# Kernel optimization log

Measured on AMD Instinct MI355X. Metric: run time of the kernel, lower is better.

The kernel has to match this reference:

```python
import jax, jax.numpy as jnp
import numpy as np

B, S, D, H, FF = 4, 1024, 1024, 16, 4096
HD = D // H
SCALE = float(np.sqrt(HD))
LAMBDA_MIN = 0.5
LAMBDA_MAX = 0.5
EPS = 1e-5


def _layernorm(x, g, b):
    mu = jnp.mean(x, axis=-1, keepdims=True)
    var = jnp.mean(jnp.square(x - mu), axis=-1, keepdims=True)
    return (x - mu) * jax.lax.rsqrt(var + EPS) * g + b


def _qbnn_layer(h, W, bW, J, lam_base, g, be):
    # s_prev = tanh(h); h_tilde = h W + b; delta_j = (sum_i s_prev_i J_ij) * tanh(h_tilde)_j
    s_prev = jnp.tanh(h)
    h_tilde = h @ W + bW
    s_raw = jnp.tanh(h_tilde)
    delta = (s_prev @ J) * s_raw
    lam_n = jax.nn.sigmoid(lam_base)
    dynamic_factor = 0.5  # eval mode, call_count=0 -> 0.5+0.5*sin(0)
    lam_eff = LAMBDA_MIN + (LAMBDA_MAX - LAMBDA_MIN) * (lam_n * 0.7 + dynamic_factor * 0.3)
    h_hat = h_tilde + lam_eff * delta
    return jax.nn.gelu(_layernorm(h_hat, g, be), approximate=False)


def setup_inputs() -> dict:
    key = jax.random.key(0)
    ks = jax.random.split(key, 24)
    f32 = jnp.float32
    lin = lambda k, i, o: jax.random.normal(k, (i, o), f32) / np.sqrt(i)
    inp = {
        'x': jax.random.normal(ks[0], (B, S, D), f32),
        # attention projections (stored as [in, out]; y = x @ W + b)
        'wq': lin(ks[1], D, D), 'bq': jnp.zeros((D,), f32),
        'wk': lin(ks[2], D, D), 'bk': jnp.zeros((D,), f32),
        'wv': lin(ks[3], D, D), 'bv': jnp.zeros((D,), f32),
        'wo': lin(ks[4], D, D), 'bo': jnp.zeros((D,), f32),
        'J_attn': jax.random.normal(ks[5], (H, HD, HD), f32) * 0.02,
        'lambda_attn': jnp.asarray(0.5, f32),
        'g_attn': jnp.ones((D,), f32), 'b_attn': jnp.zeros((D,), f32),
        # ffn layer 1 (D -> FF)
        'W1': lin(ks[6], D, FF), 'b1': jnp.zeros((FF,), f32),
        'J1': jax.random.normal(ks[7], (D, FF), f32) * 0.02,
        'lam1': jnp.asarray(0.5, f32),
        'g1': jnp.ones((FF,), f32), 'be1': jnp.zeros((FF,), f32),
        # ffn layer 2 (FF -> D)
        'W2': lin(ks[8], FF, D), 'b2': jnp.zeros((D,), f32),
        'J2': jax.random.normal(ks[9], (FF, D), f32) * 0.02,
        'lam2': jnp.asarray(0.5, f32),
        'g2': jnp.ones((D,), f32), 'be2': jnp.zeros((D,), f32),
        # ffn pre-norm
        'g_ffn': jnp.ones((D,), f32), 'b_ffn': jnp.zeros((D,), f32),
    }
    return inp


def reference(x, wq, bq, wk, bk, wv, bv, wo, bo, J_attn, lambda_attn, g_attn, b_attn,
              W1, b1, J1, lam1, g1, be1, W2, b2, J2, lam2, g2, be2, g_ffn, b_ffn):
    # --- attention (pre-norm) ---
    xn = _layernorm(x, g_attn, b_attn)
    split = lambda t: t.reshape(B, S, H, HD).transpose(0, 2, 1, 3)  # bshd -> bhsd
    Q = split(xn @ wq + bq)
    K = split(xn @ wk + bk)
    V = split(xn @ wv + bv)
    scores = jnp.einsum('bhid,bhjd->bhij', Q, K) / SCALE
    tQJ = jnp.einsum('bhid,hde->bhie', jnp.tanh(Q), J_attn)
    delta = jnp.einsum('bhie,bhje->bhij', tQJ, jnp.tanh(K))
    probs = jax.nn.softmax(scores + lambda_attn * delta, axis=-1)
    attn = jnp.einsum('bhij,bhjd->bhid', probs, V)
    attn = attn.transpose(0, 2, 1, 3).reshape(B, S, D) @ wo + bo
    x = x + attn
    # --- QBNN FFN (pre-norm) ---
    h = _layernorm(x, g_ffn, b_ffn)
    h = _qbnn_layer(h, W1, b1, J1, lam1, g1, be1)
    h = _qbnn_layer(h, W2, b2, J2, lam2, g2, be2)
    return x + h
```

## Files before the change

### kernel.cpp

```cpp
#include <hip/hip_runtime.h>
#include <cmath>

typedef unsigned short u16;
typedef unsigned int   u32;
typedef short bhalf8 __attribute__((ext_vector_type(8)));
typedef float fx4    __attribute__((ext_vector_type(4)));

#define B_   4
#define S_   1024
#define D_   1024
#define H_   16
#define HD_  64
#define FF_  4096
#define NTOK (B_*S_)
#define QKVW 3072

__device__ __forceinline__ float b2f(u16 u) {
    u32 x = ((u32)u) << 16;
    return __uint_as_float(x);
}
__device__ __forceinline__ u16 f2b(float f) {
    u32 u = __float_as_uint(f);
    u32 r = (u + 0x7fffu + ((u >> 16) & 1u)) >> 16;
    return (u16)r;
}
__device__ __forceinline__ float ftanh(float x) {
    float e = __expf(2.f * x);
    return 1.f - 2.f / (e + 1.f);
}

#define GLDS16(g, l) __builtin_amdgcn_global_load_lds( \
    (const __attribute__((address_space(1))) void*)(g), \
    (__attribute__((address_space(3))) void*)(l), 16, 0, 0)

template <int N> __device__ __forceinline__ void waitvm() {
    if constexpr (N == 8) asm volatile("s_waitcnt vmcnt(8)" ::: "memory");
    else if constexpr (N == 6) asm volatile("s_waitcnt vmcnt(6)" ::: "memory");
    else if constexpr (N == 4) asm volatile("s_waitcnt vmcnt(4)" ::: "memory");
    else if constexpr (N == 3) asm volatile("s_waitcnt vmcnt(3)" ::: "memory");
    else if constexpr (N == 2) asm volatile("s_waitcnt vmcnt(2)" ::: "memory");
    else asm volatile("s_waitcnt vmcnt(0)" ::: "memory");
}

__device__ __forceinline__ void tile_swz(int gx, int gy, int& bx, int& by) {
    int bid = blockIdx.x;
    int nwg = gx * gy;
    if (((nwg | gy) & 7) == 0) {
        int chunk = nwg >> 3;
        int wg = (bid & 7) * chunk + (bid >> 3);
        int tps = gx << 3;
        int sup = wg / tps, rem = wg % tps;
        bx = rem >> 3;
        by = (sup << 3) + (rem & 7);
    } else {
        bx = bid % gx; by = bid / gx;
    }
}

__global__ __launch_bounds__(256) void cvt_t_k(const float* __restrict__ w0, const float* __restrict__ w1,
                                               const float* __restrict__ w2, const float* __restrict__ w3,
                                               const float* __restrict__ W1p, const float* __restrict__ J1p,
                                               const float* __restrict__ W2p, const float* __restrict__ J2p,
                                               u16* __restrict__ dst) {
    __shared__ u16 L[64][65];
    int bid = blockIdx.x, tid = threadIdx.x;
    const float* src; size_t dbase; int Kd, Nd, tk, tn;
    if (bid < 1024)      { int m = bid >> 8, t = bid & 255;
                           src = m == 0 ? w0 : m == 1 ? w1 : m == 2 ? w2 : w3;
                           dbase = (size_t)m << 20; Kd = 1024; Nd = 1024; tk = t >> 4; tn = t & 15; }
    else if (bid < 2048) { int t = bid - 1024; src = W1p; dbase = (size_t)4  << 20; Kd = 1024; Nd = 4096; tk = t >> 6; tn = t & 63; }
    else if (bid < 3072) { int t = bid - 2048; src = J1p; dbase = (size_t)8  << 20; Kd = 1024; Nd = 4096; tk = t >> 6; tn = t & 63; }
    else if (bid < 4096) { int t = bid - 3072; src = W2p; dbase = (size_t)12 << 20; Kd = 4096; Nd = 1024; tk = t >> 4; tn = t & 15; }
    else                 { int t = bid - 4096; src = J2p; dbase = (size_t)16 << 20; Kd = 4096; Nd = 1024; tk = t >> 4; tn = t & 15; }
    int k0 = tk * 64, n0 = tn * 64;
    int r = tid >> 2, c4 = (tid & 3) * 16;
    #pragma unroll
    for (int p = 0; p < 4; ++p) {
        float4 v = *(const float4*)&src[(size_t)(k0 + r) * Nd + n0 + c4 + p * 4];
        L[r][c4 + p * 4 + 0] = f2b(v.x);
        L[r][c4 + p * 4 + 1] = f2b(v.y);
        L[r][c4 + p * 4 + 2] = f2b(v.z);
        L[r][c4 + p * 4 + 3] = f2b(v.w);
    }
    __syncthreads();
    u16 o[16];
    #pragma unroll
    for (int j = 0; j < 16; ++j) o[j] = L[c4 + j][r];
    *(uint4*)&dst[dbase + (size_t)(n0 + r) * Kd + k0 + c4]     = *(uint4*)&o[0];
    *(uint4*)&dst[dbase + (size_t)(n0 + r) * Kd + k0 + c4 + 8] = *(uint4*)&o[8];
}

__global__ __launch_bounds__(256) void tanh_k(const u16* __restrict__ in, u16* __restrict__ outb) {
    size_t idx = ((size_t)blockIdx.x * 256 + threadIdx.x) * 8;
    uint4 v = *(const uint4*)&in[idx];
    const u16* p = (const u16*)&v;
    u16 o[8];
    #pragma unroll
    for (int j = 0; j < 8; ++j) o[j] = f2b(ftanh(b2f(p[j])));
    *(uint4*)&outb[idx] = *(uint4*)o;
}

template <int BM, int BN, int WM, int WN, int EPI, bool SEG>
__global__ __launch_bounds__(512, 2) void gemmP(const u16* __restrict__ A,
                                                const u16* __restrict__ Bt,
                                                const float* __restrict__ bA,
                                                const float* __restrict__ bB,
                                                const float* __restrict__ bC,
                                                const float* __restrict__ resid,
                                                void* __restrict__ Cout,
                                                int M, int N, int K) {
    constexpr int IA = BM / 128;
    constexpr int IB = BN / 128;
    constexpr int NWN = BN / WN;
    constexpr int FM = WM / 16, FN = WN / 16;
    __shared__ u16 As[3][BM * 32];
    __shared__ u16 Bs[3][BN * 32];

    const int tid = threadIdx.x;
    const int w = tid >> 6, ln = tid & 63;
    const int q = ln >> 4, mr = ln & 15;
    const int wmi = w / NWN, wni = w % NWN;
    int bx, by;
    tile_swz(N / BN, M / BM, bx, by);
    const int m0 = by * BM, n0 = bx * BN;

    const int lr = ln >> 2;
    const int sc = 8 * ((ln & 3) ^ ((ln >> 3) & 3));
    const int qx8 = 8 * (q ^ ((mr >> 1) & 3));

    const u16* aA[IA];
    const u16* aB[IB];
    #pragma unroll
    for (int i = 0; i < IA; ++i)
        aA[i] = A + (size_t)(m0 + 16 * (w + 8 * i) + lr) * K + sc;
    #pragma unroll
    for (int i = 0; i < IB; ++i)
        aB[i] = Bt + (size_t)(n0 + 16 * (w + 8 * i) + lr) * K + sc;

    fx4 acc[FM][FN];
    #pragma unroll
    for (int i = 0; i < FM; ++i)
        #pragma unroll
        for (int j = 0; j < FN; ++j) acc[i][j] = (fx4){0.f, 0.f, 0.f, 0.f};

#define GP_STAGE(slot, kk) do { \
        _Pragma("unroll") \
        for (int i = 0; i < IA; ++i) GLDS16(aA[i] + (kk), &As[slot][(16 * (w + 8 * i)) * 32]); \
        _Pragma("unroll") \
        for (int i = 0; i < IB; ++i) GLDS16(aB[i] + (kk), &Bs[slot][(16 * (w + 8 * i)) * 32]); \
    } while (0)

    const int NT = K >> 5;
    GP_STAGE(0, 0);
    GP_STAGE(1, 32);
    int sl = 0, st = 2;
    for (int t = 0; t < NT; ++t) {
        if (t + 2 < NT) {
            GP_STAGE(st, (t + 2) << 5);
            waitvm<2 * (IA + IB)>();
        } else if (t + 1 < NT) {
            waitvm<IA + IB>();
        } else {
            waitvm<0>();
        }
        __builtin_amdgcn_sched_barrier(0);
        __builtin_amdgcn_s_barrier();
        __builtin_amdgcn_sched_barrier(0);

        bhalf8 afr[FM], bfr[FN];
        const u16* Ap = &As[sl][0];
        const u16* Bp = &Bs[sl][0];
        #pragma unroll
        for (int fm = 0; fm < FM; ++fm)
            afr[fm] = *(const bhalf8*)&Ap[(wmi * WM + fm * 16 + mr) * 32 + qx8];
        #pragma unroll
        for (int fn = 0; fn < FN; ++fn)
            bfr[fn] = *(const bhalf8*)&Bp[(wni * WN + fn * 16 + mr) * 32 + qx8];
        asm volatile("s_waitcnt lgkmcnt(0)" ::: "memory");
        __builtin_amdgcn_sched_barrier(0);
        __builtin_amdgcn_s_barrier();
        __builtin_amdgcn_sched_barrier(0);

        __builtin_amdgcn_s_setprio(1);
        #pragma unroll
        for (int fm = 0; fm < FM; ++fm)
            #pragma unroll
            for (int fn = 0; fn < FN; ++fn)
                acc[fm][fn] = __builtin_amdgcn_mfma_f32_16x16x32_bf16(afr[fm], bfr[fn], acc[fm][fn], 0, 0, 0);
        __builtin_amdgcn_s_setprio(0);

        sl = sl == 2 ? 0 : sl + 1;
        st = st == 2 ? 0 : st + 1;
    }
#undef GP_STAGE

    #pragma unroll
    for (int fn = 0; fn < FN; ++fn) {
        int col = n0 + wni * WN + fn * 16 + mr;
        float bs;
        if (SEG) {
            const float* bp = col < 1024 ? bA : (col < 2048 ? bB : bC);
            bs = bp[col & 1023];
        } else {
            bs = bA ? bA[col] : 0.f;
        }
        #pragma unroll
        for (int fm = 0; fm < FM; ++fm) {
            #pragma unroll
            for (int r = 0; r < 4; ++r) {
                int row    = m0 + wmi * WM + fm * 16 + q * 4 + r;
                size_t idx = (size_t)row * N + col;
                float v    = acc[fm][fn][r] + bs;
                if (EPI == 0) {
                    ((u16*)Cout)[idx] = f2b(v);
                } else if (EPI == 1) {
                    ((float*)Cout)[idx] = v + resid[idx];
                } else {
                    float ht = b2f(((u16*)Cout)[idx]);
                    ((u16*)Cout)[idx] = f2b(ht + 0.5f * v * ftanh(ht));
                }
            }
        }
    }
}

__global__ __launch_bounds__(256) void ln_k(const float* __restrict__ xin,
                                            const float* __restrict__ g,
                                            const float* __restrict__ bb,
                                            u16* __restrict__ out, int W) {
    __shared__ float red[8], red2[8], stats[2];
    int row = blockIdx.x, tid = threadIdx.x;
    float s = 0.f, ss = 0.f;
    for (int c = tid; c < W; c += 256) {
        float v = xin[(size_t)row * W + c];
        s += v; ss += v * v;
    }
    #pragma unroll
    for (int off = 32; off; off >>= 1) { s += __shfl_xor(s, off); ss += __shfl_xor(ss, off); }
    int wave = tid >> 6, lane = tid & 63;
    if (lane == 0) { red[wave] = s; red2[wave] = ss; }
    __syncthreads();
    if (tid == 0) {
        float S = 0.f, SS = 0.f;
        for (int w2 = 0; w2 < 4; ++w2) { S += red[w2]; SS += red2[w2]; }
        float mu = S / W;
        stats[0] = mu;
        stats[1] = rsqrtf(SS / W - mu * mu + 1e-5f);
    }
    __syncthreads();
    float mu = stats[0], rs = stats[1];
    for (int c = tid; c < W; c += 256)
        out[(size_t)row * W + c] = f2b((xin[(size_t)row * W + c] - mu) * rs * g[c] + bb[c]);
}

template <bool RES, bool OUT_F32>
__global__ __launch_bounds__(256) void lngelu_k(const u16* __restrict__ u,
                                                const float* __restrict__ g,
                                                const float* __restrict__ be,
                                                const float* __restrict__ resid,
                                                void* __restrict__ out, int W) {
    __shared__ float ub[4096];
    __shared__ float red[8], red2[8], stats[2];
    int row = blockIdx.x, tid = threadIdx.x;
    float s = 0.f, ss = 0.f;
    for (int c = tid; c < W; c += 256) {
        float v = b2f(u[(size_t)row * W + c]);
        ub[c] = v; s += v; ss += v * v;
    }
    #pragma unroll
    for (int off = 32; off; off >>= 1) { s += __shfl_xor(s, off); ss += __shfl_xor(ss, off); }
    int wave = tid >> 6, lane = tid & 63;
    if (lane == 0) { red[wave] = s; red2[wave] = ss; }
    __syncthreads();
    if (tid == 0) {
        float S = 0.f, SS = 0.f;
        for (int w2 = 0; w2 < 4; ++w2) { S += red[w2]; SS += red2[w2]; }
        float mu = S / W;
        stats[0] = mu;
        stats[1] = rsqrtf(SS / W - mu * mu + 1e-5f);
    }
    __syncthreads();
    float mu = stats[0], rs = stats[1];
    for (int c = tid; c < W; c += 256) {
        float v = (ub[c] - mu) * rs * g[c] + be[c];
        float y = 0.5f * v * (1.f + erff(v * 0.70710678118654752f));
        if (RES) y += resid[(size_t)row * W + c];
        if (OUT_F32) ((float*)out)[(size_t)row * W + c] = y;
        else         ((u16*)out)[(size_t)row * W + c] = f2b(y);
    }
}

__global__ __launch_bounds__(256) void aug_q_k(const u16* __restrict__ QKV,
                                               const float* __restrict__ J,
                                               const float* __restrict__ lamp,
                                               u16* __restrict__ QA) {
    __shared__ float Jl[64][68];
    __shared__ float Tq[64][65];
    int blk = blockIdx.x;
    int bh = blk >> 4, st = blk & 15;
    int b = bh >> 4, h = bh & 15;
    int s0 = st * 64;
    int tid = threadIdx.x;
    float lam = lamp[0];

    for (int i = tid; i < 4096; i += 256)
        Jl[i >> 6][i & 63] = J[h * 4096 + i];
    for (int i = tid; i < 4096; i += 256) {
        int r = i >> 6, c = i & 63;
        float v  = b2f(QKV[(size_t)(b * S_ + s0 + r) * QKVW + h * 64 + c]);
        Tq[r][c] = ftanh(v);
        QA[((size_t)(bh * S_ + s0 + r)) * 128 + c] = f2b(v * 0.125f);
    }
    __syncthreads();

    int r = tid >> 2, c0 = (tid & 3) * 16;
    float acc[16];
    #pragma unroll
    for (int j = 0; j < 16; ++j) acc[j] = 0.f;
    for (int k = 0; k < 64; ++k) {
        float a = Tq[r][k];
        #pragma unroll
        for (int j4 = 0; j4 < 4; ++j4) {
            float4 jv = *(const float4*)&Jl[k][c0 + j4 * 4];
            acc[j4 * 4 + 0] += a * jv.x;
            acc[j4 * 4 + 1] += a * jv.y;
            acc[j4 * 4 + 2] += a * jv.z;
            acc[j4 * 4 + 3] += a * jv.w;
        }
    }
    size_t orow = ((size_t)(bh * S_ + s0 + r)) * 128 + 64 + c0;
    #pragma unroll
    for (int j = 0; j < 16; ++j) QA[orow + j] = f2b(lam * acc[j]);
}

__global__ __launch_bounds__(256) void aug_k_k(const u16* __restrict__ QKV,
                                               u16* __restrict__ KA) {
    int idx = blockIdx.x * 256 + threadIdx.x;
    int d = idx & (D_ - 1);
    int bs = idx >> 10;
    int h = d >> 6, hd = d & 63;
    int b = bs >> 10, si = bs & (S_ - 1);
    u16 v      = QKV[(size_t)bs * QKVW + 1024 + d];
    size_t row = (size_t)((b * H_ + h) * S_ + si);
    KA[row * 128 + hd]      = v;
    KA[row * 128 + 64 + hd] = f2b(ftanh(b2f(v)));
}

#define QS_STRIDE 136
#define PS_STRIDE 72
__global__ __launch_bounds__(256) void attn_k(const u16* __restrict__ QA,
                                              const u16* __restrict__ KA,
                                              const u16* __restrict__ QKV,
                                              u16* __restrict__ out) {
    __shared__ u16 Qs[64 * QS_STRIDE];
    __shared__ u16 Ks[64 * QS_STRIDE];
    __shared__ u16 Vt[64 * PS_STRIDE];
    __shared__ u16 Ps[4 * 16 * PS_STRIDE];

    const int tid  = threadIdx.x;
    const int w    = tid >> 6, lane = tid & 63;
    const int q    = lane >> 4, mr = lane & 15;
    const int bh   = blockIdx.x >> 4;
    const int qt   = blockIdx.x & 15;
    const int b    = bh >> 4, h = bh & 15;

    #pragma unroll
    for (int p = 0; p < 4; ++p) {
        int idx = p * 2048 + tid * 8;
        int row = idx >> 7, col = idx & 127;
        uint4 v4 = *(const uint4*)&QA[((size_t)(bh * S_ + qt * 64 + row)) * 128 + col];
        *(uint4*)&Qs[row * QS_STRIDE + col] = v4;
    }

    fx4 zero = {0.f, 0.f, 0.f, 0.f};
    fx4 O[4] = {zero, zero, zero, zero};
    float m[4]  = {-3e38f, -3e38f, -3e38f, -3e38f};
    float l[4]  = {0.f, 0.f, 0.f, 0.f};

    for (int kt = 0; kt < 16; ++kt) {
        #pragma unroll
        for (int p = 0; p < 4; ++p) {
            int idx = p * 2048 + tid * 8;
            int row = idx >> 7, col = idx & 127;
            uint4 v4 = *(const uint4*)&KA[((size_t)(bh * S_ + kt * 64 + row)) * 128 + col];
            *(uint4*)&Ks[row * QS_STRIDE + col] = v4;
        }
        #pragma unroll
        for (int p = 0; p < 2; ++p) {
            int idx = p * 2048 + tid * 8;
            int key = idx >> 6, d0 = idx & 63;
            uint4 v4 = *(const uint4*)&QKV[((size_t)(b * S_ + kt * 64 + key)) * QKVW + 2048 + h * 64 + d0];
            const u16* vp = (const u16*)&v4;
            #pragma unroll
            for (int j = 0; j < 8; ++j) Vt[(d0 + j) * PS_STRIDE + key] = vp[j];
        }
        __syncthreads();

        fx4 St[4] = {zero, zero, zero, zero};
        bhalf8 afr[4];
        #pragma unroll
        for (int ks = 0; ks < 4; ++ks)
            afr[ks] = *(const bhalf8*)&Qs[(w * 16 + mr) * QS_STRIDE + ks * 32 + q * 8];
        __builtin_amdgcn_s_setprio(1);
        #pragma unroll
        for (int nt = 0; nt < 4; ++nt) {
            #pragma unroll
            for (int ks = 0; ks < 4; ++ks) {
                bhalf8 bf = *(const bhalf8*)&Ks[(nt * 16 + mr) * QS_STRIDE + ks * 32 + q * 8];
                St[nt] = __builtin_amdgcn_mfma_f32_16x16x32_bf16(afr[ks], bf, St[nt], 0, 0, 0);
            }
        }
        __builtin_amdgcn_s_setprio(0);

        float alpha[4];
        #pragma unroll
        for (int r = 0; r < 4; ++r) {
            float mx = fmaxf(fmaxf(St[0][r], St[1][r]), fmaxf(St[2][r], St[3][r]));
            #pragma unroll
            for (int off = 8; off; off >>= 1) mx = fmaxf(mx, __shfl_xor(mx, off));
            float nm = fmaxf(m[r], mx);
            alpha[r] = __expf(m[r] - nm);
            m[r] = nm;
            float ps = 0.f;
            #pragma unroll
            for (int nt = 0; nt < 4; ++nt) {
                float p = __expf(St[nt][r] - nm);
                St[nt][r] = p;
                ps += p;
            }
            #pragma unroll
            for (int off = 8; off; off >>= 1) ps += __shfl_xor(ps, off);
            l[r] = l[r] * alpha[r] + ps;
        }
        #pragma unroll
        for (int nt = 0; nt < 4; ++nt) {
            #pragma unroll
            for (int r = 0; r < 4; ++r) {
                Ps[(w * 16 + q * 4 + r) * PS_STRIDE + nt * 16 + mr] = f2b(St[nt][r]);
                O[nt][r] *= alpha[r];
            }
        }

        __builtin_amdgcn_s_setprio(1);
        #pragma unroll
        for (int ks = 0; ks < 2; ++ks) {
            bhalf8 pa = *(const bhalf8*)&Ps[(w * 16 + mr) * PS_STRIDE + ks * 32 + q * 8];
            #pragma unroll
            for (int nt = 0; nt < 4; ++nt) {
                bhalf8 bf = *(const bhalf8*)&Vt[(nt * 16 + mr) * PS_STRIDE + ks * 32 + q * 8];
                O[nt] = __builtin_amdgcn_mfma_f32_16x16x32_bf16(pa, bf, O[nt], 0, 0, 0);
            }
        }
        __builtin_amdgcn_s_setprio(0);
        __syncthreads();
    }

    #pragma unroll
    for (int nt = 0; nt < 4; ++nt) {
        int d = nt * 16 + mr;
        #pragma unroll
        for (int r = 0; r < 4; ++r) {
            int row = qt * 64 + w * 16 + q * 4 + r;
            out[((size_t)(b * S_ + row)) * D_ + h * 64 + d] = f2b(O[nt][r] / l[r]);
        }
    }
}

extern "C" void kernel_launch(void* const* d_in, const int* in_sizes, int n_in,
                              void* d_out, int out_size, void* d_ws, size_t ws_size,
                              hipStream_t stream) {
    const float* x      = (const float*)d_in[0];
    const float* wq     = (const float*)d_in[1];
    const float* bq     = (const float*)d_in[2];
    const float* wk     = (const float*)d_in[3];
    const float* bk     = (const float*)d_in[4];
    const float* wv     = (const float*)d_in[5];
    const float* bv     = (const float*)d_in[6];
    const float* wo     = (const float*)d_in[7];
    const float* bo     = (const float*)d_in[8];
    const float* Jattn  = (const float*)d_in[9];
    const float* lamA   = (const float*)d_in[10];
    const float* g_attn = (const float*)d_in[11];
    const float* b_attn = (const float*)d_in[12];
    const float* W1     = (const float*)d_in[13];
    const float* b1     = (const float*)d_in[14];
    const float* J1     = (const float*)d_in[15];
    const float* g1     = (const float*)d_in[17];
    const float* be1    = (const float*)d_in[18];
    const float* W2     = (const float*)d_in[19];
    const float* b2     = (const float*)d_in[20];
    const float* J2     = (const float*)d_in[21];
    const float* g2     = (const float*)d_in[23];
    const float* be2    = (const float*)d_in[24];
    const float* g_ffn  = (const float*)d_in[25];
    const float* b_ffn  = (const float*)d_in[26];
    float* out = (float*)d_out;
    (void)in_sizes; (void)n_in; (void)out_size; (void)ws_size;

    char* wsp = (char*)d_ws;
    const size_t MB = 1u << 20;
    u16* WB = (u16*)(wsp);
    const u16* qkvT = WB;
    const u16* woT  = WB + ((size_t)3 << 20);
    const u16* W1T  = WB + ((size_t)4 << 20);
    const u16* J1T  = WB + ((size_t)8 << 20);
    const u16* W2T  = WB + ((size_t)12 << 20);
    const u16* J2T  = WB + ((size_t)16 << 20);
    u16*   XN   = (u16*)(wsp + 40 * MB);
    u16*   AT   = (u16*)(wsp + 40 * MB);
    u16*   U2   = (u16*)(wsp + 40 * MB);
    u16*   QKVb = (u16*)(wsp + 48 * MB);
    u16*   Hb   = (u16*)(wsp + 48 * MB);
    float* X2   = (float*)(wsp + 56 * MB);
    u16*   QA   = (u16*)(wsp + 72 * MB);
    u16*   KA   = (u16*)(wsp + 88 * MB);
    u16*   U1   = (u16*)(wsp + 72 * MB);

    dim3 blk(256), blk5(512);
    cvt_t_k<<<5120, blk, 0, stream>>>(wq, wk, wv, wo, W1, J1, W2, J2, WB);
    ln_k<<<NTOK, blk, 0, stream>>>(x, g_attn, b_attn, XN, D_);
    gemmP<128, 256, 64, 64, 0, true><<<(QKVW / 256) * (NTOK / 128), blk5, 0, stream>>>(
        XN, qkvT, bq, bk, bv, nullptr, QKVb, NTOK, QKVW, D_);
    aug_q_k<<<B_ * H_ * (S_ / 64), blk, 0, stream>>>(QKVb, Jattn, lamA, QA);
    aug_k_k<<<(NTOK * D_) / 256, blk, 0, stream>>>(QKVb, KA);
    attn_k<<<B_ * H_ * (S_ / 64), blk, 0, stream>>>(QA, KA, QKVb, AT);
    gemmP<128, 128, 64, 32, 1, false><<<(D_ / 128) * (NTOK / 128), blk5, 0, stream>>>(
        AT, woT, bo, nullptr, nullptr, x, X2, NTOK, D_, D_);
    ln_k<<<NTOK, blk, 0, stream>>>(X2, g_ffn, b_ffn, Hb, D_);
    gemmP<256, 256, 128, 64, 0, false><<<(FF_ / 256) * (NTOK / 256), blk5, 0, stream>>>(
        Hb, W1T, b1, nullptr, nullptr, nullptr, U1, NTOK, FF_, D_);
    tanh_k<<<(NTOK * D_) / 2048, blk, 0, stream>>>(Hb, Hb);
    gemmP<256, 256, 128, 64, 2, false><<<(FF_ / 256) * (NTOK / 256), blk5, 0, stream>>>(
        Hb, J1T, nullptr, nullptr, nullptr, nullptr, U1, NTOK, FF_, D_);
    lngelu_k<false, false><<<NTOK, blk, 0, stream>>>(U1, g1, be1, nullptr, U1, FF_);
    gemmP<128, 128, 64, 32, 0, false><<<(D_ / 128) * (NTOK / 128), blk5, 0, stream>>>(
        U1, W2T, b2, nullptr, nullptr, nullptr, U2, NTOK, D_, FF_);
    tanh_k<<<(NTOK * FF_) / 2048, blk, 0, stream>>>(U1, U1);
    gemmP<128, 128, 64, 32, 2, false><<<(D_ / 128) * (NTOK / 128), blk5, 0, stream>>>(
        U1, J2T, nullptr, nullptr, nullptr, nullptr, U2, NTOK, D_, FF_);
    lngelu_k<true, true><<<NTOK, blk, 0, stream>>>(U2, g2, be2, X2, out, D_);
}
```

Measured before the change: 716.7 us.

## Pipeline attention K/V loads, pre-transpose V, retile GEMMs and use 4-slot buffers

The GEMM moves from three to four LDS slots and issues its fragment reads after the barrier, which removes one barrier per k-step. A new vt_k kernel writes V pre-transposed so attention can stream K and V with swizzled async global-to-LDS loads, double-buffered against compute. Q fragments are hoisted out of the attention key loop. The QKV and FFN1 GEMMs switch to 128x128 tiles for more blocks at lower per-block reuse, and the change adds an extra kernel launch and an extra pass over V.

```diff
diff --git a/kernel.cpp b/kernel.cpp
--- a/kernel.cpp
+++ b/kernel.cpp
@@ -113,8 +113,8 @@
     constexpr int IB = BN / 128;
     constexpr int NWN = BN / WN;
     constexpr int FM = WM / 16, FN = WN / 16;
-    __shared__ u16 As[3][BM * 32];
-    __shared__ u16 Bs[3][BN * 32];
+    __shared__ u16 As[4][BM * 32];
+    __shared__ u16 Bs[4][BN * 32];
 
     const int tid = threadIdx.x;
     const int w = tid >> 6, ln = tid & 63;
@@ -153,34 +153,31 @@
     const int NT = K >> 5;
     GP_STAGE(0, 0);
     GP_STAGE(1, 32);
-    int sl = 0, st = 2;
     for (int t = 0; t < NT; ++t) {
         if (t + 2 < NT) {
-            GP_STAGE(st, (t + 2) << 5);
+            GP_STAGE((t + 2) & 3, (t + 2) << 5);
             waitvm<2 * (IA + IB)>();
         } else if (t + 1 < NT) {
             waitvm<IA + IB>();
         } else {
             waitvm<0>();
         }
-        __builtin_amdgcn_sched_barrier(0);
-        __builtin_amdgcn_s_barrier();
-        __builtin_amdgcn_sched_barrier(0);
-
-        bhalf8 afr[FM], bfr[FN];
-        const u16* Ap = &As[sl][0];
-        const u16* Bp = &Bs[sl][0];
-        #pragma unroll
-        for (int fm = 0; fm < FM; ++fm)
-            afr[fm] = *(const bhalf8*)&Ap[(wmi * WM + fm * 16 + mr) * 32 + qx8];
-        #pragma unroll
-        for (int fn = 0; fn < FN; ++fn)
-            bfr[fn] = *(const bhalf8*)&Bp[(wni * WN + fn * 16 + mr) * 32 + qx8];
         asm volatile("s_waitcnt lgkmcnt(0)" ::: "memory");
         __builtin_amdgcn_sched_barrier(0);
         __builtin_amdgcn_s_barrier();
         __builtin_amdgcn_sched_barrier(0);
 
+        const int sl = t & 3;
+        bhalf8 afr[FM], bfr[FN];
+        const u16* Ap = &As[sl][0];
+        const u16* Bp = &Bs[sl][0];
+        #pragma unroll
+        for (int fm = 0; fm < FM; ++fm)
+            afr[fm] = *(const bhalf8*)&Ap[(wmi * WM + fm * 16 + mr) * 32 + qx8];
+        #pragma unroll
+        for (int fn = 0; fn < FN; ++fn)
+            bfr[fn] = *(const bhalf8*)&Bp[(wni * WN + fn * 16 + mr) * 32 + qx8];
+
         __builtin_amdgcn_s_setprio(1);
         #pragma unroll
         for (int fm = 0; fm < FM; ++fm)
@@ -188,9 +185,6 @@
             for (int fn = 0; fn < FN; ++fn)
                 acc[fm][fn] = __builtin_amdgcn_mfma_f32_16x16x32_bf16(afr[fm], bfr[fn], acc[fm][fn], 0, 0, 0);
         __builtin_amdgcn_s_setprio(0);
-
-        sl = sl == 2 ? 0 : sl + 1;
-        st = st == 2 ? 0 : st + 1;
     }
 #undef GP_STAGE
 
@@ -346,23 +340,49 @@
     KA[row * 128 + 64 + hd] = f2b(ftanh(b2f(v)));
 }
 
+__global__ __launch_bounds__(256) void vt_k(const u16* __restrict__ QKV,
+                                            u16* __restrict__ VT) {
+    __shared__ u16 L[64][72];
+    int blk = blockIdx.x;
+    int bh = blk >> 4, st = blk & 15;
+    int b = bh >> 4, h = bh & 15;
+    int s0 = st * 64;
+    int tid = threadIdx.x;
+    #pragma unroll
+    for (int p = 0; p < 2; ++p) {
+        int i = p * 2048 + tid * 8;
+        int r = i >> 6, c = i & 63;
+        uint4 v = *(const uint4*)&QKV[((size_t)(b * S_ + s0 + r)) * QKVW + 2048 + h * 64 + c];
+        *(uint4*)&L[r][c] = v;
+    }
+    __syncthreads();
+    #pragma unroll
+    for (int p = 0; p < 2; ++p) {
+        int i = p * 2048 + tid * 8;
+        int d = i >> 6, s = i & 63;
+        u16 o[8];
+        #pragma unroll
+        for (int j = 0; j < 8; ++j) o[j] = L[s + j][d];
+        *(uint4*)&VT[((size_t)(bh * 64 + d)) * S_ + s0 + s] = *(uint4*)o;
+    }
+}
+
 #define QS_STRIDE 136
 #define PS_STRIDE 72
 __global__ __launch_bounds__(256) void attn_k(const u16* __restrict__ QA,
                                               const u16* __restrict__ KA,
-                                              const u16* __restrict__ QKV,
+                                              const u16* __restrict__ VT,
                                               u16* __restrict__ out) {
     __shared__ u16 Qs[64 * QS_STRIDE];
-    __shared__ u16 Ks[64 * QS_STRIDE];
-    __shared__ u16 Vt[64 * PS_STRIDE];
-    __shared__ u16 Ps[4 * 16 * PS_STRIDE];
+    __shared__ u16 Ks[2][64 * 128];
+    __shared__ u16 Vs[2][64 * 64];
+    __shared__ u16 Ps[64 * PS_STRIDE];
 
     const int tid  = threadIdx.x;
     const int w    = tid >> 6, lane = tid & 63;
     const int q    = lane >> 4, mr = lane & 15;
     const int bh   = blockIdx.x >> 4;
     const int qt   = blockIdx.x & 15;
-    const int b    = bh >> 4, h = bh & 15;
 
     #pragma unroll
     for (int p = 0; p < 4; ++p) {
@@ -372,41 +392,53 @@
         *(uint4*)&Qs[row * QS_STRIDE + col] = v4;
     }
 
+#define STAGEKV(pp, kt) do { \
+        _Pragma("unroll") \
+        for (int i = 0; i < 4; ++i) { \
+            int R = w * 16 + i * 4 + (lane >> 4); \
+            GLDS16(KA + ((size_t)(bh * S_ + (kt) * 64 + R)) * 128 + 8 * ((lane & 15) ^ (R & 7)), \
+                   &Ks[pp][(w * 16 + i * 4) * 128]); \
+        } \
+        _Pragma("unroll") \
+        for (int i = 0; i < 2; ++i) { \
+            int Rv = w * 16 + i * 8 + (lane >> 3); \
+            GLDS16(VT + ((size_t)(bh * 64 + Rv)) * S_ + (kt) * 64 + 8 * ((lane & 7) ^ (Rv & 7)), \
+                   &Vs[pp][(w * 16 + i * 8) * 64]); \
+        } \
+    } while (0)
+
+    STAGEKV(0, 0);
+    __syncthreads();
+
+    bhalf8 afr[4];
+    #pragma unroll
+    for (int ks = 0; ks < 4; ++ks)
+        afr[ks] = *(const bhalf8*)&Qs[(w * 16 + mr) * QS_STRIDE + ks * 32 + q * 8];
+
     fx4 zero = {0.f, 0.f, 0.f, 0.f};
     fx4 O[4] = {zero, zero, zero, zero};
     float m[4]  = {-3e38f, -3e38f, -3e38f, -3e38f};
     float l[4]  = {0.f, 0.f, 0.f, 0.f};
 
+    int p = 0;
     for (int kt = 0; kt < 16; ++kt) {
-        #pragma unroll
-        for (int p = 0; p < 4; ++p) {
-            int idx = p * 2048 + tid * 8;
-            int row = idx >> 7, col = idx & 127;
-            uint4 v4 = *(const uint4*)&KA[((size_t)(bh * S_ + kt * 64 + row)) * 128 + col];
-            *(uint4*)&Ks[row * QS_STRIDE + col] = v4;
-        }
-        #pragma unroll
-        for (int p = 0; p < 2; ++p) {
-            int idx = p * 2048 + tid * 8;
-            int key = idx >> 6, d0 = idx & 63;
-            uint4 v4 = *(const uint4*)&QKV[((size_t)(b * S_ + kt * 64 + key)) * QKVW + 2048 + h * 64 + d0];
-            const u16* vp = (const u16*)&v4;
-            #pragma unroll
-            for (int j = 0; j < 8; ++j) Vt[(d0 + j) * PS_STRIDE + key] = vp[j];
-        }
-        __syncthreads();
+        if (kt + 1 < 16) {
+            STAGEKV(p ^ 1, kt + 1);
+            waitvm<6>();
+        } else {
+            waitvm<0>();
+        }
+        __builtin_amdgcn_sched_barrier(0);
+        __builtin_amdgcn_s_barrier();
+        __builtin_amdgcn_sched_barrier(0);
 
         fx4 St[4] = {zero, zero, zero, zero};
-        bhalf8 afr[4];
-        #pragma unroll
-        for (int ks = 0; ks < 4; ++ks)
-            afr[ks] = *(const bhalf8*)&Qs[(w * 16 + mr) * QS_STRIDE + ks * 32 + q * 8];
         __builtin_amdgcn_s_setprio(1);
         #pragma unroll
         for (int nt = 0; nt < 4; ++nt) {
             #pragma unroll
             for (int ks = 0; ks < 4; ++ks) {
-                bhalf8 bf = *(const bhalf8*)&Ks[(nt * 16 + mr) * QS_STRIDE + ks * 32 + q * 8];
+                bhalf8 bf = *(const bhalf8*)&Ks[p][(nt * 16 + mr) * 128 + 8 * (((ks * 4 + q) ^ (mr & 7)))];
                 St[nt] = __builtin_amdgcn_mfma_f32_16x16x32_bf16(afr[ks], bf, St[nt], 0, 0, 0);
             }
         }
@@ -424,9 +456,9 @@
             float ps = 0.f;
             #pragma unroll
             for (int nt = 0; nt < 4; ++nt) {
-                float p = __expf(St[nt][r] - nm);
-                St[nt][r] = p;
-                ps += p;
+                float pv = __expf(St[nt][r] - nm);
+                St[nt][r] = pv;
+                ps += pv;
             }
             #pragma unroll
             for (int off = 8; off; off >>= 1) ps += __shfl_xor(ps, off);
@@ -447,14 +479,19 @@
             bhalf8 pa = *(const bhalf8*)&Ps[(w * 16 + mr) * PS_STRIDE + ks * 32 + q * 8];
             #pragma unroll
             for (int nt = 0; nt < 4; ++nt) {
-                bhalf8 bf = *(const bhalf8*)&Vt[(nt * 16 + mr) * PS_STRIDE + ks * 32 + q * 8];
+                bhalf8 bf = *(const bhalf8*)&Vs[p][(nt * 16 + mr) * 64 + 8 * (((ks * 4 + q) ^ (mr & 7)))];
                 O[nt] = __builtin_amdgcn_mfma_f32_16x16x32_bf16(pa, bf, O[nt], 0, 0, 0);
             }
         }
         __builtin_amdgcn_s_setprio(0);
-        __syncthreads();
-    }
-
+        asm volatile("s_waitcnt lgkmcnt(0)" ::: "memory");
+        __builtin_amdgcn_sched_barrier(0);
+        __builtin_amdgcn_s_barrier();
+        p ^= 1;
+    }
+#undef STAGEKV
+
+    const int b = bh >> 4, h = bh & 15;
     #pragma unroll
     for (int nt = 0; nt < 4; ++nt) {
         int d = nt * 16 + mr;
@@ -515,22 +552,24 @@
     u16*   QA   = (u16*)(wsp + 72 * MB);
     u16*   KA   = (u16*)(wsp + 88 * MB);
     u16*   U1   = (u16*)(wsp + 72 * MB);
+    u16*   VT   = (u16*)(wsp + 104 * MB);
 
     dim3 blk(256), blk5(512);
     cvt_t_k<<<5120, blk, 0, stream>>>(wq, wk, wv, wo, W1, J1, W2, J2, WB);
     ln_k<<<NTOK, blk, 0, stream>>>(x, g_attn, b_attn, XN, D_);
-    gemmP<128, 256, 64, 64, 0, true><<<(QKVW / 256) * (NTOK / 128), blk5, 0, stream>>>(
+    gemmP<128, 128, 64, 32, 0, true><<<(QKVW / 128) * (NTOK / 128), blk5, 0, stream>>>(
         XN, qkvT, bq, bk, bv, nullptr, QKVb, NTOK, QKVW, D_);
     aug_q_k<<<B_ * H_ * (S_ / 64), blk, 0, stream>>>(QKVb, Jattn, lamA, QA);
     aug_k_k<<<(NTOK * D_) / 256, blk, 0, stream>>>(QKVb, KA);
-    attn_k<<<B_ * H_ * (S_ / 64), blk, 0, stream>>>(QA, KA, QKVb, AT);
+    vt_k<<<B_ * H_ * (S_ / 64), blk, 0, stream>>>(QKVb, VT);
+    attn_k<<<B_ * H_ * (S_ / 64), blk, 0, stream>>>(QA, KA, VT, AT);
     gemmP<128, 128, 64, 32, 1, false><<<(D_ / 128) * (NTOK / 128), blk5, 0, stream>>>(
         AT, woT, bo, nullptr, nullptr, x, X2, NTOK, D_, D_);
     ln_k<<<NTOK, blk, 0, stream>>>(X2, g_ffn, b_ffn, Hb, D_);
-    gemmP<256, 256, 128, 64, 0, false><<<(FF_ / 256) * (NTOK / 256), blk5, 0, stream>>>(
+    gemmP<128, 128, 64, 32, 0, false><<<(FF_ / 128) * (NTOK / 128), blk5, 0, stream>>>(
         Hb, W1T, b1, nullptr, nullptr, nullptr, U1, NTOK, FF_, D_);
     tanh_k<<<(NTOK * D_) / 2048, blk, 0, stream>>>(Hb, Hb);
-    gemmP<256, 256, 128, 64, 2, false><<<(FF_ / 256) * (NTOK / 256), blk5, 0, stream>>>(
+    gemmP<128, 128, 64, 32, 2, false><<<(FF_ / 128) * (NTOK / 128), blk5, 0, stream>>>(
         Hb, J1T, nullptr, nullptr, nullptr, nullptr, U1, NTOK, FF_, D_);
     lngelu_k<false, false><<<NTOK, blk, 0, stream>>>(U1, g1, be1, nullptr, U1, FF_);
     gemmP<128, 128, 64, 32, 0, false><<<(D_ / 128) * (NTOK / 128), blk5, 0, stream>>>(
```

Result: faster. 656.8 us (-8.4%).
